# Kernel optimization log

Measured on AMD Instinct MI355X. Metric: run time of the kernel, lower is better.

The kernel has to match this reference:

```python
import jax, jax.numpy as jnp
import numpy as np

B, T, SIG, MET, H, F, OUT = 256, 128, 64, 32, 256, 16, 1
TWO_PI = float(2.0 * np.pi)


def setup_inputs() -> dict:
    key = jax.random.key(0)
    ks = jax.random.split(key, 24)
    rn = lambda k, s, sc=0.05: jax.random.normal(k, s, jnp.float32) * sc
    return {
        "signal": rn(ks[0], (B, T, SIG), 1.0),
        "metmast": rn(ks[1], (B, T, MET), 1.0),
        "W_i_signal": rn(ks[2], (SIG, H)),
        "W_ste_signal": rn(ks[3], (SIG, H)),
        "W_fre_signal": rn(ks[4], (SIG, F)),
        "W_c_signal": rn(ks[5], (SIG, H)),
        "W_o_signal": rn(ks[6], (SIG, H)),
        "W_i_metmast": rn(ks[7], (MET, H)),
        "W_ste_metmast": rn(ks[8], (MET, H)),
        "W_fre_metmast": rn(ks[9], (MET, F)),
        "W_c_metmast": rn(ks[10], (MET, H)),
        "W_o_metmast": rn(ks[11], (MET, H)),
        "U_i": rn(ks[12], (H, H)),
        "b_i": jnp.zeros((H,), jnp.float32),
        "U_ste": rn(ks[13], (H, H)),
        "b_ste": jnp.ones((H,), jnp.float32),
        "U_fre": rn(ks[14], (H, F)),
        "b_fre": jnp.ones((F,), jnp.float32),
        "U_c": rn(ks[15], (H, H)),
        "b_c": jnp.zeros((H,), jnp.float32),
        "U_o": rn(ks[16], (H, H)),
        "b_o": jnp.zeros((H,), jnp.float32),
        "U_a": rn(ks[17], (F, 1)),
        "b_a": jnp.zeros((H,), jnp.float32),
        "W_p": rn(ks[18], (H, OUT)),
        "b_p": jnp.zeros((OUT,), jnp.float32),
        "fc_w": rn(ks[19], (OUT, OUT), 0.5),
        "fc_b": jnp.zeros((OUT,), jnp.float32),
    }


def _hsig(x):
    # torch.nn.Hardsigmoid: clip(x/6 + 0.5, 0, 1)
    return jnp.clip(x / 6.0 + 0.5, 0.0, 1.0)


def reference(signal, metmast, W_i_signal, W_ste_signal, W_fre_signal, W_c_signal,
              W_o_signal, W_i_metmast, W_ste_metmast, W_fre_metmast, W_c_metmast,
              W_o_metmast, U_i, b_i, U_ste, b_ste, U_fre, b_fre, U_c, b_c, U_o, b_o,
              U_a, b_a, W_p, b_p, fc_w, fc_b):
    Bn, Tn, _ = signal.shape
    Hn, Fn = U_i.shape[0], U_a.shape[0]
    freq = jnp.arange(Fn, dtype=jnp.float32) / Fn  # [F]
    sig_t = jnp.swapaxes(signal, 0, 1)   # [T, B, SIG]
    met_t = jnp.swapaxes(metmast, 0, 1)  # [T, B, MET]

    def step(carry, x):
        h, S_re, S_im, t = carry
        xs, xm = x
        x_i = xs @ W_i_signal + xm @ W_i_metmast + b_i
        x_ste = xs @ W_ste_signal + xm @ W_ste_metmast + b_ste
        x_fre = xs @ W_fre_signal + xm @ W_fre_metmast + b_fre
        x_c = xs @ W_c_signal + xm @ W_c_metmast + b_c
        x_o = xs @ W_o_signal + xm @ W_o_metmast + b_o
        i = _hsig(x_i + h @ U_i)                # [B,H]
        ste = _hsig(x_ste + h @ U_ste)          # [B,H]
        fre = _hsig(x_fre + h @ U_fre)          # [B,F]
        f = ste[:, :, None] * fre[:, None, :]   # [B,H,F] forget gate
        c = i * jnp.tanh(x_c + h @ U_c)         # [B,H]
        t = t + 1.0
        omega = TWO_PI * t * freq               # [F]
        re, im = jnp.cos(omega), jnp.sin(omega)
        c3 = c[:, :, None]
        S_re = f * S_re + c3 * re
        S_im = f * S_im + c3 * im
        A = S_re * S_re + S_im * S_im           # [B,H,F] amplitude
        A_a = jnp.einsum('bhf,f->bh', A, U_a[:, 0])
        a = jnp.tanh(A_a + b_a)
        o = _hsig(x_o + h @ U_o)
        h = o * a
        return (h, S_re, S_im, t), None

    S0 = jnp.zeros((Bn, Hn, Fn), jnp.float32)
    carry0 = (jnp.zeros((Bn, Hn), jnp.float32), S0, S0, jnp.float32(0.0))
    (h, _, _, _), _ = jax.lax.scan(step, carry0, (sig_t, met_t))
    p = h @ W_p + b_p                # [B, OUT] (last timestep only is used)
    out = p @ fc_w.T + fc_b          # fc_out
    return out.squeeze()
```

## Files before the change

kernel.cpp:

```cpp
#include <hip/hip_runtime.h>
#include <hip/hip_fp16.h>
#include <cstdint>
#include <cstddef>

#define B_    256
#define T_    128
#define SIG_  64
#define MET_  32
#define H_    256
#define F_    16
#define NCOL  1040

__device__ __forceinline__ float hsig(float x) {
    return fminf(fmaxf(x * (1.0f/6.0f) + 0.5f, 0.0f), 1.0f);
}

__device__ __forceinline__ unsigned short f2h(float f) {
    __half h = __float2half(f);
    return *(unsigned short*)&h;
}

__device__ __forceinline__ float ntload_f(const float* p) {
    return __builtin_nontemporal_load(p);
}
__device__ __forceinline__ float4 ntload_f4(const float* p) {
    float4 v;
    v.x = __builtin_nontemporal_load(p + 0);
    v.y = __builtin_nontemporal_load(p + 1);
    v.z = __builtin_nontemporal_load(p + 2);
    v.w = __builtin_nontemporal_load(p + 3);
    return v;
}

typedef _Float16 half2v __attribute__((ext_vector_type(2)));

__device__ __forceinline__ float dot2(unsigned int u, unsigned int h, float acc) {
#if __has_builtin(__builtin_amdgcn_fdot2)
    return __builtin_amdgcn_fdot2(__builtin_bit_cast(half2v, u),
                                  __builtin_bit_cast(half2v, h), acc, false);
#else
    __half2 uu = *(__half2*)&u, hh = *(__half2*)&h;
    float2 uf = __half22float2(uu), hf = __half22float2(hh);
    return fmaf(uf.x, hf.x, fmaf(uf.y, hf.y, acc));
#endif
}

__global__ __launch_bounds__(256) void pack_kernel(
    const float* __restrict__ Wis, const float* __restrict__ Wstes, const float* __restrict__ Wfres,
    const float* __restrict__ Wcs, const float* __restrict__ Wos,
    const float* __restrict__ Wim, const float* __restrict__ Wstem, const float* __restrict__ Wfrem,
    const float* __restrict__ Wcm, const float* __restrict__ Wom,
    const float* __restrict__ Ui, const float* __restrict__ Uste, const float* __restrict__ Ufre,
    const float* __restrict__ Uc, const float* __restrict__ Uo,
    const float* __restrict__ bi, const float* __restrict__ bste, const float* __restrict__ bfre,
    const float* __restrict__ bc, const float* __restrict__ bo,
    float* __restrict__ Wcat, float* __restrict__ bcat,
    unsigned short* __restrict__ U8, unsigned short* __restrict__ UF)
{
    int gtid = blockIdx.x * blockDim.x + threadIdx.x;
    int stride = gridDim.x * blockDim.x;
    const float* Wsig[5] = {Wis, Wstes, Wcs, Wos, Wfres};
    const float* Wmet[5] = {Wim, Wstem, Wcm, Wom, Wfrem};
    const float* Us[4]   = {Ui, Uste, Uc, Uo};
    const float* bs[5]   = {bi, bste, bc, bo, bfre};

    for (int i = gtid; i < 96*NCOL; i += stride) {
        int k = i / NCOL, n = i - k*NCOL;
        int sec, idx, secN;
        if (n < 1024) { sec = n >> 8; idx = n & 255; secN = H_; }
        else          { sec = 4; idx = n - 1024; secN = F_; }
        float v = (k < 64) ? Wsig[sec][k*secN + idx] : Wmet[sec][(k-64)*secN + idx];
        Wcat[k*NCOL + n] = v;
    }
    for (int n = gtid; n < NCOL; n += stride) {
        int sec, idx;
        if (n < 1024) { sec = n >> 8; idx = n & 255; }
        else          { sec = 4; idx = n - 1024; }
        bcat[n] = bs[sec][idx];
    }
    for (int i = gtid; i < 1024*H_; i += stride) {
        int col = i >> 8, k = i & 255;
        int sec = col >> 8, idx = col & 255;
        float v = Us[sec][k*H_ + idx];
        U8[(((k >> 3) * 1024) + col) * 8 + (k & 7)] = f2h(v);
    }
    for (int i = gtid; i < 16*H_; i += stride) {
        int col = i >> 8, k = i & 255;
        UF[col*H_ + k] = f2h(Ufre[k*F_ + col]);
    }
}

__global__ __launch_bounds__(256) void proj_kernel(
    const float* __restrict__ sig, const float* __restrict__ met,
    const float* __restrict__ Wcat, const float* __restrict__ bcat,
    float* __restrict__ X)
{
    __shared__ float A_s[32][128];
    __shared__ float W_s[32][128];
    int tid = threadIdx.x;
    int c0b = blockIdx.x * 128;
    int m0  = blockIdx.y * 128;
    int t0  = blockIdx.z * 16;
    int r0  = (tid >> 4) * 8;
    int c0t = (tid & 15) * 8;

    float acc[8][8];
    #pragma unroll
    for (int i = 0; i < 8; ++i)
        #pragma unroll
        for (int j = 0; j < 8; ++j) acc[i][j] = 0.0f;

    for (int k0 = 0; k0 < 96; k0 += 32) {
        for (int idx = tid; idx < 32*128; idx += 256) {
            int ml = idx & 127, kk = idx >> 7;
            int m = m0 + ml;
            int b = m >> 4, tl = m & 15;
            int g = b * T_ + t0 + tl;
            int k = k0 + kk;
            float v = (k < 64) ? sig[g*SIG_ + k] : met[g*MET_ + (k - 64)];
            A_s[kk][ml] = v;
        }
        for (int idx = tid; idx < 32*128; idx += 256) {
            int c = idx & 127, kk = idx >> 7;
            int n = c0b + c;
            W_s[kk][c] = (n < NCOL) ? Wcat[(k0+kk)*NCOL + n] : 0.0f;
        }
        __syncthreads();
        #pragma unroll
        for (int kk = 0; kk < 32; ++kk) {
            float4 a0 = *(const float4*)&A_s[kk][r0];
            float4 a1 = *(const float4*)&A_s[kk][r0+4];
            float4 w0 = *(const float4*)&W_s[kk][c0t];
            float4 w1 = *(const float4*)&W_s[kk][c0t+4];
            float av[8] = {a0.x,a0.y,a0.z,a0.w,a1.x,a1.y,a1.z,a1.w};
            float wv[8] = {w0.x,w0.y,w0.z,w0.w,w1.x,w1.y,w1.z,w1.w};
            #pragma unroll
            for (int i = 0; i < 8; ++i)
                #pragma unroll
                for (int j = 0; j < 8; ++j)
                    acc[i][j] = fmaf(av[i], wv[j], acc[i][j]);
        }
        __syncthreads();
    }
    #pragma unroll
    for (int i = 0; i < 8; ++i) {
        int m = m0 + r0 + i;
        int bb = m >> 4, tl = m & 15;
        size_t row = (size_t)bb * T_ + t0 + tl;
        #pragma unroll
        for (int j = 0; j < 8; ++j) {
            int n = c0b + c0t + j;
            if (n < NCOL) X[row*NCOL + n] = acc[i][j] + bcat[n];
        }
    }
}

__global__ __launch_bounds__(1024, 4) void recur_kernel(
    const float* __restrict__ X, const uint4* __restrict__ U8,
    const uint4* __restrict__ UF,
    const float* __restrict__ U_a, const float* __restrict__ b_a,
    const float* __restrict__ W_p, const float* __restrict__ b_p,
    const float* __restrict__ fc_w, const float* __restrict__ fc_b,
    float* __restrict__ out)
{
    __shared__ unsigned int h_p[H_/2];
    __shared__ float pre_s[1024];
    __shared__ float qp[64];
    __shared__ float cs_s[16], sn_s[16];

    int tid  = threadIdx.x;
    int b    = blockIdx.x;
    int lane = tid & 63;
    int wid  = tid >> 6;
    bool isfre = ((lane & 15) == 15);
    int fq = lane >> 4;

    int j  = tid >> 2;
    int f0 = (tid & 3) * 4;

    if (tid < H_/2) h_p[tid] = 0u;
    if (tid < 16) {
        float ang = (float)tid * 0.39269908169872414f;
        cs_s[tid] = cosf(ang);
        sn_s[tid] = sinf(ang);
    }
    float Sre[4], Sim[4];
    #pragma unroll
    for (int r = 0; r < 4; ++r) { Sre[r] = 0.0f; Sim[r] = 0.0f; }

    float ba_j = b_a[j];
    float4 ua4 = ((const float4*)U_a)[tid & 3];
    const uint4* Uf = UF + (wid * 32 + fq * 8);
    const float* Xb = X + (size_t)b * T_ * NCOL;
    __half* h_h = (__half*)h_p;

    float hnew = 0.0f;
    __syncthreads();

    for (int t = 0; t < T_; ++t) {
        const float* xrow = Xb + (size_t)t * NCOL;

        float acc = ntload_f(&xrow[tid]);
        #pragma unroll 8
        for (int kk = 0; kk < 32; ++kk) {
            uint4 u  = U8[kk * 1024 + tid];
            uint4 hp = *(const uint4*)&h_p[kk * 4];
            acc = dot2(u.x, hp.x, acc);
            acc = dot2(u.y, hp.y, acc);
            acc = dot2(u.z, hp.z, acc);
            acc = dot2(u.w, hp.w, acc);
        }
        float fa = 0.0f;
        if (isfre) {
            #pragma unroll
            for (int q = 0; q < 8; ++q) {
                uint4 u  = Uf[q];
                uint4 hp = *(const uint4*)&h_p[fq * 32 + q * 4];
                fa = dot2(u.x, hp.x, fa);
                fa = dot2(u.y, hp.y, fa);
                fa = dot2(u.z, hp.z, fa);
                fa = dot2(u.w, hp.w, fa);
            }
        }
        pre_s[tid] = acc;
        if (isfre) qp[wid*4 + fq] = fa;
        __syncthreads();

        float xi   = pre_s[j];
        float xste = pre_s[256 + j];
        float xc   = pre_s[512 + j];
        float xo   = pre_s[768 + j];
        float gi   = hsig(xi);
        float gste = hsig(xste);
        float go   = hsig(xo);
        float cc   = gi * tanhf(xc);

        float4 xfre = ntload_f4(&xrow[1024 + f0]);
        float4 q0 = *(const float4*)&qp[(f0+0)*4];
        float4 q1 = *(const float4*)&qp[(f0+1)*4];
        float4 q2 = *(const float4*)&qp[(f0+2)*4];
        float4 q3 = *(const float4*)&qp[(f0+3)*4];
        float fre[4];
        fre[0] = hsig(xfre.x + q0.x + q0.y + q0.z + q0.w);
        fre[1] = hsig(xfre.y + q1.x + q1.y + q1.z + q1.w);
        fre[2] = hsig(xfre.z + q2.x + q2.y + q2.z + q2.w);
        fre[3] = hsig(xfre.w + q3.x + q3.y + q3.z + q3.w);

        int tt1 = (t + 1) & 15;
        float Aa = 0.0f;
        #pragma unroll
        for (int r = 0; r < 4; ++r) {
            int idx = (tt1 * (f0 + r)) & 15;
            float dec = gste * fre[r];
            float sre = fmaf(dec, Sre[r], cc * cs_s[idx]);
            float sim = fmaf(dec, Sim[r], cc * sn_s[idx]);
            Sre[r] = sre; Sim[r] = sim;
            Aa = fmaf(fmaf(sre, sre, sim*sim), ((const float*)&ua4)[r], Aa);
        }
        Aa += __shfl_xor(Aa, 1);
        Aa += __shfl_xor(Aa, 2);
        if ((tid & 3) == 0) {
            float a = tanhf(Aa + ba_j);
            hnew = go * a;
            h_h[j] = __float2half(hnew);
        }
        __syncthreads();
    }

    if ((tid & 3) == 0) pre_s[j] = hnew * W_p[j];
    __syncthreads();
    for (int s = 128; s > 0; s >>= 1) {
        if (tid < s) pre_s[tid] += pre_s[tid + s];
        __syncthreads();
    }
    if (tid == 0) out[b] = (pre_s[0] + b_p[0]) * fc_w[0] + fc_b[0];
}

extern "C" void kernel_launch(void* const* d_in, const int* in_sizes, int n_in,
                              void* d_out, int out_size, void* d_ws, size_t ws_size,
                              hipStream_t stream) {
    const float* signal = (const float*)d_in[0];
    const float* metmast = (const float*)d_in[1];
    const float* W_i_s   = (const float*)d_in[2];
    const float* W_ste_s = (const float*)d_in[3];
    const float* W_fre_s = (const float*)d_in[4];
    const float* W_c_s   = (const float*)d_in[5];
    const float* W_o_s   = (const float*)d_in[6];
    const float* W_i_m   = (const float*)d_in[7];
    const float* W_ste_m = (const float*)d_in[8];
    const float* W_fre_m = (const float*)d_in[9];
    const float* W_c_m   = (const float*)d_in[10];
    const float* W_o_m   = (const float*)d_in[11];
    const float* U_i   = (const float*)d_in[12];
    const float* b_i   = (const float*)d_in[13];
    const float* U_ste = (const float*)d_in[14];
    const float* b_ste = (const float*)d_in[15];
    const float* U_fre = (const float*)d_in[16];
    const float* b_fre = (const float*)d_in[17];
    const float* U_c   = (const float*)d_in[18];
    const float* b_c   = (const float*)d_in[19];
    const float* U_o   = (const float*)d_in[20];
    const float* b_o   = (const float*)d_in[21];
    const float* U_a   = (const float*)d_in[22];
    const float* b_a   = (const float*)d_in[23];
    const float* W_p   = (const float*)d_in[24];
    const float* b_p   = (const float*)d_in[25];
    const float* fc_w  = (const float*)d_in[26];
    const float* fc_b  = (const float*)d_in[27];
    float* out = (float*)d_out;

    char* ws = (char*)d_ws;
    float*          Wcat = (float*)(ws + 0);
    float*          bcat = (float*)(ws + 399360);
    unsigned short* U8   = (unsigned short*)(ws + 403520);
    unsigned short* UF   = (unsigned short*)(ws + 927808);
    float*          X    = (float*)(ws + 936000);

    pack_kernel<<<256, 256, 0, stream>>>(
        W_i_s, W_ste_s, W_fre_s, W_c_s, W_o_s,
        W_i_m, W_ste_m, W_fre_m, W_c_m, W_o_m,
        U_i, U_ste, U_fre, U_c, U_o,
        b_i, b_ste, b_fre, b_c, b_o,
        Wcat, bcat, U8, UF);

    proj_kernel<<<dim3(9, 32, 8), 256, 0, stream>>>(signal, metmast, Wcat, bcat, X);

    recur_kernel<<<B_, 1024, 0, stream>>>(X, (const uint4*)U8, (const uint4*)UF,
                                          U_a, b_a, W_p, b_p, fc_w, fc_b, out);
}
```

Baseline: 1.097 ms.

## Split recurrent weights across registers, LDS and global memory

```diff
diff --git a/kernel.cpp b/kernel.cpp
--- a/kernel.cpp
+++ b/kernel.cpp
@@ -10,6 +10,13 @@
 #define H_    256
 #define F_    16
 #define NCOL  1040
+
+#define KREG 112
+#define KLDS 24
+#define NREG4 14
+#define NLDSD 12
+#define NGLB4 15
+#define LSTR  13
 
 __device__ __forceinline__ float hsig(float x) {
     return fminf(fmaxf(x * (1.0f/6.0f) + 0.5f, 0.0f), 1.0f);
@@ -55,7 +62,8 @@
     const float* __restrict__ bi, const float* __restrict__ bste, const float* __restrict__ bfre,
     const float* __restrict__ bc, const float* __restrict__ bo,
     float* __restrict__ Wcat, float* __restrict__ bcat,
-    unsigned short* __restrict__ U8, unsigned short* __restrict__ UF)
+    unsigned short* __restrict__ UR, unsigned short* __restrict__ UL,
+    unsigned short* __restrict__ UG, unsigned short* __restrict__ UF)
 {
     int gtid = blockIdx.x * blockDim.x + threadIdx.x;
     int stride = gridDim.x * blockDim.x;
@@ -81,8 +89,16 @@
     for (int i = gtid; i < 1024*H_; i += stride) {
         int col = i >> 8, k = i & 255;
         int sec = col >> 8, idx = col & 255;
-        float v = Us[sec][k*H_ + idx];
-        U8[(((k >> 3) * 1024) + col) * 8 + (k & 7)] = f2h(v);
+        unsigned short v = f2h(Us[sec][k*H_ + idx]);
+        if (k < KREG) {
+            UR[(((k >> 3) * 1024) + col) * 8 + (k & 7)] = v;
+        } else if (k < KREG + KLDS) {
+            int kd = k - KREG;
+            UL[((kd >> 1) * 1024 + col) * 2 + (kd & 1)] = v;
+        } else {
+            int kk = k - (KREG + KLDS);
+            UG[(((kk >> 3) * 1024) + col) * 8 + (kk & 7)] = v;
+        }
     }
     for (int i = gtid; i < 16*H_; i += stride) {
         int col = i >> 8, k = i & 255;
@@ -156,15 +172,17 @@
 }
 
 __global__ __launch_bounds__(1024, 4) void recur_kernel(
-    const float* __restrict__ X, const uint4* __restrict__ U8,
-    const uint4* __restrict__ UF,
+    const float* __restrict__ X,
+    const uint4* __restrict__ URg, const unsigned int* __restrict__ ULg,
+    const uint4* __restrict__ UGg, const uint4* __restrict__ UF,
     const float* __restrict__ U_a, const float* __restrict__ b_a,
     const float* __restrict__ W_p, const float* __restrict__ b_p,
     const float* __restrict__ fc_w, const float* __restrict__ fc_b,
     float* __restrict__ out)
 {
+    __shared__ unsigned int ldsU[1024 * LSTR];
+    __shared__ float pre_s[1024];
     __shared__ unsigned int h_p[H_/2];
-    __shared__ float pre_s[1024];
     __shared__ float qp[64];
     __shared__ float cs_s[16], sn_s[16];
 
@@ -178,6 +196,14 @@
     int j  = tid >> 2;
     int f0 = (tid & 3) * 4;
 
+    uint4 ureg[NREG4];
+    #pragma unroll
+    for (int i = 0; i < NREG4; ++i) ureg[i] = URg[i * 1024 + tid];
+
+    #pragma unroll
+    for (int d = 0; d < NLDSD; ++d)
+        ldsU[tid * LSTR + d] = ULg[d * 1024 + tid];
+
     if (tid < H_/2) h_p[tid] = 0u;
     if (tid < 16) {
         float ang = (float)tid * 0.39269908169872414f;
@@ -200,16 +226,32 @@
     for (int t = 0; t < T_; ++t) {
         const float* xrow = Xb + (size_t)t * NCOL;
 
-        float acc = ntload_f(&xrow[tid]);
-        #pragma unroll 8
-        for (int kk = 0; kk < 32; ++kk) {
-            uint4 u  = U8[kk * 1024 + tid];
-            uint4 hp = *(const uint4*)&h_p[kk * 4];
-            acc = dot2(u.x, hp.x, acc);
-            acc = dot2(u.y, hp.y, acc);
-            acc = dot2(u.z, hp.z, acc);
-            acc = dot2(u.w, hp.w, acc);
-        }
+        float acc0 = ntload_f(&xrow[tid]);
+        float acc1 = 0.0f, acc2 = 0.0f;
+
+        #pragma unroll
+        for (int g = 0; g < NGLB4; ++g) {
+            uint4 u  = UGg[g * 1024 + tid];
+            uint4 hp = *(const uint4*)&h_p[(KREG + KLDS)/2 + g*4];
+            acc2 = dot2(u.x, hp.x, acc2);
+            acc2 = dot2(u.y, hp.y, acc2);
+            acc2 = dot2(u.z, hp.z, acc2);
+            acc2 = dot2(u.w, hp.w, acc2);
+        }
+        #pragma unroll
+        for (int i = 0; i < NREG4; ++i) {
+            uint4 hp = *(const uint4*)&h_p[i*4];
+            acc0 = dot2(ureg[i].x, hp.x, acc0);
+            acc0 = dot2(ureg[i].y, hp.y, acc0);
+            acc0 = dot2(ureg[i].z, hp.z, acc0);
+            acc0 = dot2(ureg[i].w, hp.w, acc0);
+        }
+        #pragma unroll
+        for (int d = 0; d < NLDSD; ++d)
+            acc1 = dot2(ldsU[tid * LSTR + d], h_p[KREG/2 + d], acc1);
+
+        float acc = acc0 + acc1 + acc2;
+
         float fa = 0.0f;
         if (isfre) {
             #pragma unroll
@@ -312,7 +354,9 @@
     char* ws = (char*)d_ws;
     float*          Wcat = (float*)(ws + 0);
     float*          bcat = (float*)(ws + 399360);
-    unsigned short* U8   = (unsigned short*)(ws + 403520);
+    unsigned short* UR   = (unsigned short*)(ws + 403520);
+    unsigned short* UL   = (unsigned short*)(ws + 632896);
+    unsigned short* UG   = (unsigned short*)(ws + 682048);
     unsigned short* UF   = (unsigned short*)(ws + 927808);
     float*          X    = (float*)(ws + 936000);
 
@@ -321,10 +365,12 @@
         W_i_m, W_ste_m, W_fre_m, W_c_m, W_o_m,
         U_i, U_ste, U_fre, U_c, U_o,
         b_i, b_ste, b_fre, b_c, b_o,
-        Wcat, bcat, U8, UF);
+        Wcat, bcat, UR, UL, UG, UF);
 
     proj_kernel<<<dim3(9, 32, 8), 256, 0, stream>>>(signal, metmast, Wcat, bcat, X);
 
-    recur_kernel<<<B_, 1024, 0, stream>>>(X, (const uint4*)U8, (const uint4*)UF,
+    recur_kernel<<<B_, 1024, 0, stream>>>(X,
+                                          (const uint4*)UR, (const unsigned int*)UL,
+                                          (const uint4*)UG, (const uint4*)UF,
                                           U_a, b_a, W_p, b_p, fc_w, fc_b, out);
 }
```

Measured after the change: 1.781 ms. 1.62x slower.

## Cache recurrent fp16 weights in registers and LDS with 512-thread blocks

Applied to the files above, without the earlier changes.

```diff
diff --git a/kernel.cpp b/kernel.cpp
--- a/kernel.cpp
+++ b/kernel.cpp
@@ -10,6 +10,10 @@
 #define H_    256
 #define F_    16
 #define NCOL  1040
+
+#define QREG 40
+#define QLDS 7
+#define QGLB 17
 
 __device__ __forceinline__ float hsig(float x) {
     return fminf(fmaxf(x * (1.0f/6.0f) + 0.5f, 0.0f), 1.0f);
@@ -43,6 +47,14 @@
     float2 uf = __half22float2(uu), hf = __half22float2(hh);
     return fmaf(uf.x, hf.x, fmaf(uf.y, hf.y, acc));
 #endif
+}
+
+__device__ __forceinline__ float dot2x4(uint4 u, uint4 h, float acc) {
+    acc = dot2(u.x, h.x, acc);
+    acc = dot2(u.y, h.y, acc);
+    acc = dot2(u.z, h.z, acc);
+    acc = dot2(u.w, h.w, acc);
+    return acc;
 }
 
 __global__ __launch_bounds__(256) void pack_kernel(
@@ -55,7 +67,7 @@
     const float* __restrict__ bi, const float* __restrict__ bste, const float* __restrict__ bfre,
     const float* __restrict__ bc, const float* __restrict__ bo,
     float* __restrict__ Wcat, float* __restrict__ bcat,
-    unsigned short* __restrict__ U8, unsigned short* __restrict__ UF)
+    unsigned short* __restrict__ U9, unsigned short* __restrict__ UF)
 {
     int gtid = blockIdx.x * blockDim.x + threadIdx.x;
     int stride = gridDim.x * blockDim.x;
@@ -80,9 +92,11 @@
     }
     for (int i = gtid; i < 1024*H_; i += stride) {
         int col = i >> 8, k = i & 255;
-        int sec = col >> 8, idx = col & 255;
-        float v = Us[sec][k*H_ + idx];
-        U8[(((k >> 3) * 1024) + col) * 8 + (k & 7)] = f2h(v);
+        int g = col >> 8, j = col & 255;
+        int tid = ((g & 1) << 8) + j;
+        int s   = g >> 1;
+        int q   = ((k >> 3) << 1) | s;
+        U9[(q * 512 + tid) * 8 + (k & 7)] = f2h(Us[g][k*H_ + j]);
     }
     for (int i = gtid; i < 16*H_; i += stride) {
         int col = i >> 8, k = i & 255;
@@ -155,16 +169,18 @@
     }
 }
 
-__global__ __launch_bounds__(1024, 4) void recur_kernel(
-    const float* __restrict__ X, const uint4* __restrict__ U8,
+__global__ __launch_bounds__(512, 1) __attribute__((amdgpu_waves_per_eu(1, 2)))
+void recur_kernel(
+    const float* __restrict__ X, const uint4* __restrict__ U9,
     const uint4* __restrict__ UF,
     const float* __restrict__ U_a, const float* __restrict__ b_a,
     const float* __restrict__ W_p, const float* __restrict__ b_p,
     const float* __restrict__ fc_w, const float* __restrict__ fc_b,
     float* __restrict__ out)
 {
-    __shared__ unsigned int h_p[H_/2];
+    __shared__ uint4 ldsU[QLDS * 512];
     __shared__ float pre_s[1024];
+    __shared__ uint4 h_p4[H_/8];
     __shared__ float qp[64];
     __shared__ float cs_s[16], sn_s[16];
 
@@ -172,27 +188,39 @@
     int b    = blockIdx.x;
     int lane = tid & 63;
     int wid  = tid >> 6;
-    bool isfre = ((lane & 15) == 15);
-    int fq = lane >> 4;
-
-    int j  = tid >> 2;
-    int f0 = (tid & 3) * 4;
-
-    if (tid < H_/2) h_p[tid] = 0u;
+    bool isfre = ((lane & 7) == 7);
+    int fs = lane >> 3;
+    int fcol = 2*wid + (fs >> 2);
+    int fq   = fs & 3;
+
+    int j  = tid >> 1;
+    int hf = tid & 1;
+
+    uint4 ureg[QREG];
+    #pragma unroll
+    for (int q = 0; q < QREG; ++q) ureg[q] = U9[q * 512 + tid];
+
+    #pragma unroll
+    for (int d = 0; d < QLDS; ++d)
+        ldsU[d * 512 + tid] = U9[(QREG + d) * 512 + tid];
+
+    if (tid < H_/8) { uint4 z; z.x=z.y=z.z=z.w=0u; h_p4[tid] = z; }
     if (tid < 16) {
         float ang = (float)tid * 0.39269908169872414f;
         cs_s[tid] = cosf(ang);
         sn_s[tid] = sinf(ang);
     }
-    float Sre[4], Sim[4];
-    #pragma unroll
-    for (int r = 0; r < 4; ++r) { Sre[r] = 0.0f; Sim[r] = 0.0f; }
+    float Sre[8], Sim[8];
+    #pragma unroll
+    for (int r = 0; r < 8; ++r) { Sre[r] = 0.0f; Sim[r] = 0.0f; }
 
     float ba_j = b_a[j];
-    float4 ua4 = ((const float4*)U_a)[tid & 3];
-    const uint4* Uf = UF + (wid * 32 + fq * 8);
+    float4 ua_a = ((const float4*)U_a)[hf*2];
+    float4 ua_b = ((const float4*)U_a)[hf*2 + 1];
+    const uint4* Ug = U9 + (QREG + QLDS) * 512 + tid;
+    const uint4* Uf = UF + (fcol * 32 + fq * 8);
     const float* Xb = X + (size_t)b * T_ * NCOL;
-    __half* h_h = (__half*)h_p;
+    __half* h_h = (__half*)h_p4;
 
     float hnew = 0.0f;
     __syncthreads();
@@ -200,30 +228,43 @@
     for (int t = 0; t < T_; ++t) {
         const float* xrow = Xb + (size_t)t * NCOL;
 
-        float acc = ntload_f(&xrow[tid]);
-        #pragma unroll 8
-        for (int kk = 0; kk < 32; ++kk) {
-            uint4 u  = U8[kk * 1024 + tid];
-            uint4 hp = *(const uint4*)&h_p[kk * 4];
-            acc = dot2(u.x, hp.x, acc);
-            acc = dot2(u.y, hp.y, acc);
-            acc = dot2(u.z, hp.z, acc);
-            acc = dot2(u.w, hp.w, acc);
-        }
-        float fa = 0.0f;
+        float acc0 = ntload_f(&xrow[tid]);
+        float acc1 = ntload_f(&xrow[512 + tid]);
+        float accg = 0.0f;
+
+        #pragma unroll
+        for (int q = QREG + QLDS; q < 64; ++q) {
+            uint4 u  = Ug[(q - QREG - QLDS) * 512];
+            uint4 hp = *(const uint4*)&h_p4[q >> 1];
+            if (q & 1) acc1 = dot2x4(u, hp, acc1);
+            else       accg = dot2x4(u, hp, accg);
+        }
+        #pragma unroll
+        for (int c = 0; c < QREG/2; ++c) {
+            uint4 hp = h_p4[c];
+            acc0 = dot2x4(ureg[2*c],     hp, acc0);
+            acc1 = dot2x4(ureg[2*c + 1], hp, acc1);
+        }
+        #pragma unroll
+        for (int d = 0; d < QLDS; ++d) {
+            int q = QREG + d;
+            uint4 u  = ldsU[d * 512 + tid];
+            uint4 hp = h_p4[q >> 1];
+            if (q & 1) acc1 = dot2x4(u, hp, acc1);
+            else       acc0 = dot2x4(u, hp, acc0);
+        }
+        acc0 += accg;
+
         if (isfre) {
+            float fa = 0.0f;
             #pragma unroll
-            for (int q = 0; q < 8; ++q) {
-                uint4 u  = Uf[q];
-                uint4 hp = *(const uint4*)&h_p[fq * 32 + q * 4];
-                fa = dot2(u.x, hp.x, fa);
-                fa = dot2(u.y, hp.y, fa);
-                fa = dot2(u.z, hp.z, fa);
-                fa = dot2(u.w, hp.w, fa);
-            }
-        }
-        pre_s[tid] = acc;
-        if (isfre) qp[wid*4 + fq] = fa;
+            for (int i = 0; i < 8; ++i)
+                fa = dot2x4(Uf[i], h_p4[fq*8 + i], fa);
+            qp[fcol*4 + fq] = fa;
+        }
+
+        pre_s[tid]       = acc0;
+        pre_s[512 + tid] = acc1;
         __syncthreads();
 
         float xi   = pre_s[j];
@@ -235,31 +276,27 @@
         float go   = hsig(xo);
         float cc   = gi * tanhf(xc);
 
-        float4 xfre = ntload_f4(&xrow[1024 + f0]);
-        float4 q0 = *(const float4*)&qp[(f0+0)*4];
-        float4 q1 = *(const float4*)&qp[(f0+1)*4];
-        float4 q2 = *(const float4*)&qp[(f0+2)*4];
-        float4 q3 = *(const float4*)&qp[(f0+3)*4];
-        float fre[4];
-        fre[0] = hsig(xfre.x + q0.x + q0.y + q0.z + q0.w);
-        fre[1] = hsig(xfre.y + q1.x + q1.y + q1.z + q1.w);
-        fre[2] = hsig(xfre.z + q2.x + q2.y + q2.z + q2.w);
-        fre[3] = hsig(xfre.w + q3.x + q3.y + q3.z + q3.w);
+        float4 xf0 = ntload_f4(&xrow[1024 + hf*8]);
+        float4 xf1 = ntload_f4(&xrow[1024 + hf*8 + 4]);
+        float xfre[8] = {xf0.x,xf0.y,xf0.z,xf0.w,xf1.x,xf1.y,xf1.z,xf1.w};
 
         int tt1 = (t + 1) & 15;
         float Aa = 0.0f;
         #pragma unroll
-        for (int r = 0; r < 4; ++r) {
-            int idx = (tt1 * (f0 + r)) & 15;
-            float dec = gste * fre[r];
+        for (int r = 0; r < 8; ++r) {
+            int f = hf*8 + r;
+            float4 q4 = *(const float4*)&qp[f*4];
+            float fre = hsig(xfre[r] + q4.x + q4.y + q4.z + q4.w);
+            int idx = (tt1 * f) & 15;
+            float dec = gste * fre;
             float sre = fmaf(dec, Sre[r], cc * cs_s[idx]);
             float sim = fmaf(dec, Sim[r], cc * sn_s[idx]);
             Sre[r] = sre; Sim[r] = sim;
-            Aa = fmaf(fmaf(sre, sre, sim*sim), ((const float*)&ua4)[r], Aa);
+            float ua = (r < 4) ? ((const float*)&ua_a)[r] : ((const float*)&ua_b)[r-4];
+            Aa = fmaf(fmaf(sre, sre, sim*sim), ua, Aa);
         }
         Aa += __shfl_xor(Aa, 1);
-        Aa += __shfl_xor(Aa, 2);
-        if ((tid & 3) == 0) {
+        if (hf == 0) {
             float a = tanhf(Aa + ba_j);
             hnew = go * a;
             h_h[j] = __float2half(hnew);
@@ -267,7 +304,7 @@
         __syncthreads();
     }
 
-    if ((tid & 3) == 0) pre_s[j] = hnew * W_p[j];
+    if (hf == 0) pre_s[j] = hnew * W_p[j];
     __syncthreads();
     for (int s = 128; s > 0; s >>= 1) {
         if (tid < s) pre_s[tid] += pre_s[tid + s];
@@ -312,7 +349,7 @@
     char* ws = (char*)d_ws;
     float*          Wcat = (float*)(ws + 0);
     float*          bcat = (float*)(ws + 399360);
-    unsigned short* U8   = (unsigned short*)(ws + 403520);
+    unsigned short* U9   = (unsigned short*)(ws + 403520);
     unsigned short* UF   = (unsigned short*)(ws + 927808);
     float*          X    = (float*)(ws + 936000);
 
@@ -321,10 +358,10 @@
         W_i_m, W_ste_m, W_fre_m, W_c_m, W_o_m,
         U_i, U_ste, U_fre, U_c, U_o,
         b_i, b_ste, b_fre, b_c, b_o,
-        Wcat, bcat, U8, UF);
+        Wcat, bcat, U9, UF);
 
     proj_kernel<<<dim3(9, 32, 8), 256, 0, stream>>>(signal, metmast, Wcat, bcat, X);
 
-    recur_kernel<<<B_, 1024, 0, stream>>>(X, (const uint4*)U8, (const uint4*)UF,
-                                          U_a, b_a, W_p, b_p, fc_w, fc_b, out);
-}
+    recur_kernel<<<B_, 512, 0, stream>>>(X, (const uint4*)U9, (const uint4*)UF,
+                                         U_a, b_a, W_p, b_p, fc_w, fc_b, out);
+}
```

Result: slower. 3.022 ms (+175.5%).
